# Performance work log

Measured on AMD Instinct MI355X. Metric: run time of the kernel, lower is better.

## Reference

```python
import jax, jax.numpy as jnp
import numpy as np

B, D_IN, T = 16, 1024, 4096
CB_SIZE, CB_DIM = 8192, 512
EPS = 1e-12


def _conv1d_s2(x, w):
    # x: [b, c_in, t], w: [c_out, c_in, 3]; stride 2, padding 1 (matches nn.Conv1d)
    return jax.lax.conv_general_dilated(
        x, w, window_strides=(2,), padding=[(1, 1)],
        dimension_numbers=("NCH", "OIH", "NCH"))


def _l2_normalize(v):
    # F.normalize(v, dim=1) semantics
    return v / jnp.maximum(jnp.linalg.norm(v, axis=1, keepdims=True), EPS)


def setup_inputs() -> dict:
    key = jax.random.key(0)
    k1, k2, k3, k4 = jax.random.split(key, 4)
    x = jax.random.normal(k1, (B, D_IN, T), dtype=jnp.float32)
    w1 = jax.random.normal(k2, (CB_DIM, D_IN, 3), dtype=jnp.float32) * 0.02
    w2 = jax.random.normal(k3, (CB_DIM, CB_DIM, 3), dtype=jnp.float32) * 0.02
    codebook = jax.random.normal(k4, (CB_SIZE, CB_DIM), dtype=jnp.float32)
    return {"x": x, "w1": w1, "w2": w2, "codebook": codebook}


def reference(x, w1, w2, codebook):
    # in_proj: two stride-2 convs -> [b, cb_dim, t], t = T // 4
    x_e = _conv1d_s2(_conv1d_s2(x, w1), w2)
    b, d, t = x_e.shape
    enc = x_e.transpose(0, 2, 1).reshape(b * t, d)   # (b t) d
    enc = _l2_normalize(enc)
    cb = _l2_normalize(codebook)
    # squared euclidean distance via matmul
    dist = (jnp.sum(enc * enc, axis=1, keepdims=True)
            - 2.0 * enc @ cb.T
            + jnp.sum(cb * cb, axis=1)[None, :])     # (b t) codebook_size
    indices = jnp.argmax(-dist, axis=1).reshape(b, t)
    return indices
```

## Files before the change

kernel.cpp:

```cpp
#include <hip/hip_runtime.h>


typedef __attribute__((ext_vector_type(8))) _Float16 f16x8;
typedef __attribute__((ext_vector_type(8))) short bf16x8;
typedef __attribute__((ext_vector_type(4))) float f32x4;

__device__ inline ushort f2bf(float x) {
  union { float f; unsigned u; } v; v.f = x;
  unsigned r = v.u + 0x7fffu + ((v.u >> 16) & 1u);
  return (ushort)(r >> 16);
}

__device__ inline void splitf(float v, ushort& h, ushort& l) {
  union { _Float16 h; ushort u; } a, b;
  a.h = (_Float16)v;
  b.h = (_Float16)(v - (float)a.h);
  h = a.u; l = b.u;
}

__global__ __launch_bounds__(256) void prep_w(const float* __restrict__ w,
                                              ushort* __restrict__ ws,
                                              int n ) {
  const int idx = blockIdx.x * 256 + threadIdx.x;
  if (idx >= n) return;
  const float v0 = w[(size_t)idx * 3 + 0];
  const float v1 = w[(size_t)idx * 3 + 1];
  const float v2 = w[(size_t)idx * 3 + 2];
  ushort h, l;
  splitf(v0, h, l); ws[idx] = h; ws[(size_t)n + idx] = l;
  splitf(v1, h, l); ws[2 * (size_t)n + idx] = h; ws[3 * (size_t)n + idx] = l;
  splitf(v2, h, l); ws[4 * (size_t)n + idx] = h; ws[5 * (size_t)n + idx] = l;
}

__global__ __launch_bounds__(256) void zero_halo(ushort* __restrict__ xo1,
                                                 ushort* __restrict__ xo2) {
  const int b = blockIdx.x, tid = threadIdx.x;
  const uint4 z = make_uint4(0, 0, 0, 0);
  *(uint4*)(xo1 + (size_t)b * 2049 * 2048 + tid * 8) = z;
  if (tid < 128) *(uint4*)(xo2 + (size_t)b * 1025 * 1024 + tid * 8) = z;
}

template <int CI, int T>
__global__ __launch_bounds__(256) void prep_x(const float* __restrict__ x,
                                              ushort* __restrict__ xe,
                                              ushort* __restrict__ xo) {
  const int t0 = blockIdx.x * 256;
  const int ci0 = blockIdx.y * 32;
  const int b = blockIdx.z;
  const int tid = threadIdx.x;
  __shared__ float tile[32][257];
  const int wv = tid >> 6, lane = tid & 63;
  const float* xb = x + ((size_t)b * CI + ci0) * T + t0;
#pragma unroll
  for (int r = 0; r < 8; r++) {
    const int ci = r * 4 + wv;
    const float4 v = *(const float4*)(xb + (size_t)ci * T + lane * 4);
    tile[ci][lane * 4 + 0] = v.x; tile[ci][lane * 4 + 1] = v.y;
    tile[ci][lane * 4 + 2] = v.z; tile[ci][lane * 4 + 3] = v.w;
  }
  __syncthreads();
  const int jj = tid >> 1, ph = tid & 1;
  const int tl = 2 * jj + ph;
  __attribute__((aligned(16))) ushort h[32], l[32];
#pragma unroll
  for (int c = 0; c < 32; c++) splitf(tile[c][tl], h[c], l[c]);
  constexpr int TH = T / 2;
  constexpr int RW = CI * 2;
  ushort* dst;
  if (ph == 0) dst = xe + ((size_t)b * TH + (t0 >> 1) + jj) * RW;
  else dst = xo + ((size_t)b * (TH + 1) + (t0 >> 1) + jj + 1) * RW;
  dst += (ci0 >> 5) * 64;
#pragma unroll
  for (int k = 0; k < 4; k++) {
    *(uint4*)(dst + k * 8) = *(const uint4*)(h + k * 8);
    *(uint4*)(dst + 32 + k * 8) = *(const uint4*)(l + k * 8);
  }
}

template <int C_IN, int T_OUT, bool SPLIT_OUT>
__global__ __launch_bounds__(256, 4) void conv_mfma(
    const ushort* __restrict__ xe, const ushort* __restrict__ xo,
    const ushort* __restrict__ ws, float* __restrict__ out,
    ushort* __restrict__ ye, ushort* __restrict__ yo) {
  const int co0 = blockIdx.x * 128;
  const int t0 = blockIdx.y * 64;
  const int b = blockIdx.z;
  const int tid = threadIdx.x;
  const int wv = tid >> 6, lane = tid & 63;
  const int l15 = lane & 15, quad = lane >> 4;

  __shared__ ushort xeh[64 * 40], xel[64 * 40], xoh[65 * 40], xol[65 * 40];

  f32x4 acc[2][4] = {};
  const int RW = C_IN * 2;
  const ushort* xe_b = xe + ((size_t)b * T_OUT + t0) * RW;
  const ushort* xo_b = xo + ((size_t)b * (T_OUT + 1) + t0) * RW;

  for (int ci0 = 0; ci0 < C_IN; ci0 += 32) {
    __syncthreads();
    const int choff = (ci0 >> 5) * 64;
#pragma unroll
    for (int q = 0; q < 5; q++) {
      const int id = tid + 256 * q;
      if (id < 1032) {
        const int g = id & 3;
        const int u = id >> 2;
        const uint4* src;
        ushort* dst;
        if (u < 128) {
          const int row = u >> 1, part = u & 1;
          src = (const uint4*)(xe_b + (size_t)row * RW + choff + part * 32 + g * 8);
          dst = (part ? xel : xeh) + row * 40 + g * 8;
        } else {
          const int u2 = u - 128;
          const int row = u2 >> 1, part = u2 & 1;
          src = (const uint4*)(xo_b + (size_t)row * RW + choff + part * 32 + g * 8);
          dst = (part ? xol : xoh) + row * 40 + g * 8;
        }
        *(uint4*)dst = *src;
      }
    }
    __syncthreads();

#pragma unroll
    for (int koff = 0; koff < 3; koff++) {
      f16x8 a_h[2], a_l[2];
#pragma unroll
      for (int i = 0; i < 2; i++) {
        const size_t co = (size_t)co0 + wv * 32 + i * 16 + l15;
        const ushort* wp = ws + ((size_t)(koff * 2) * 512) * C_IN + co * C_IN + ci0 + quad * 8;
        a_h[i] = *(const f16x8*)wp;
        a_l[i] = *(const f16x8*)(wp + (size_t)512 * C_IN);
      }
      const ushort* bh = (koff == 1) ? xeh : xoh;
      const ushort* bl = (koff == 1) ? xel : xol;
      const int radd = (koff == 2) ? 1 : 0;
#pragma unroll
      for (int j = 0; j < 4; j++) {
        const int row = j * 16 + l15 + radd;
        const f16x8 b_h = *(const f16x8*)(bh + row * 40 + quad * 8);
        const f16x8 b_l = *(const f16x8*)(bl + row * 40 + quad * 8);
#pragma unroll
        for (int i = 0; i < 2; i++) {
          acc[i][j] = __builtin_amdgcn_mfma_f32_16x16x32_f16(a_h[i], b_h, acc[i][j], 0, 0, 0);
          acc[i][j] = __builtin_amdgcn_mfma_f32_16x16x32_f16(a_h[i], b_l, acc[i][j], 0, 0, 0);
          acc[i][j] = __builtin_amdgcn_mfma_f32_16x16x32_f16(a_l[i], b_h, acc[i][j], 0, 0, 0);
        }
      }
    }
  }

  if (SPLIT_OUT) {
#pragma unroll
    for (int i = 0; i < 2; i++) {
      const int ch = (co0 >> 5) + wv;
      const int ci32 = i * 16 + quad * 4;
#pragma unroll
      for (int j = 0; j < 4; j++) {
        const int t = t0 + j * 16 + l15;
        const int ph = t & 1;
        const int row = (t >> 1) + ph;
        __attribute__((aligned(8))) ushort h[4], l[4];
#pragma unroll
        for (int r = 0; r < 4; r++) splitf(acc[i][j][r], h[r], l[r]);
        ushort* dst = (ph ? yo : ye) +
                      ((size_t)b * (ph ? 1025 : 1024) + row) * 1024 + ch * 64 + ci32;
        *(uint2*)dst = *(const uint2*)h;
        *(uint2*)(dst + 32) = *(const uint2*)l;
      }
    }
  } else {
#pragma unroll
    for (int i = 0; i < 2; i++) {
#pragma unroll
      for (int j = 0; j < 4; j++) {
        const int t = t0 + j * 16 + l15;
        const int co = co0 + wv * 32 + i * 16 + quad * 4;
        const float4 v = make_float4(acc[i][j][0], acc[i][j][1], acc[i][j][2], acc[i][j][3]);
        *(float4*)(out + ((size_t)b * T_OUT + t) * 512 + co) = v;
      }
    }
  }
}

__global__ __launch_bounds__(64) void norm_rows(const float* __restrict__ out2t,
                                                float* __restrict__ enc,
                                                ushort* __restrict__ enc16) {
  const int row = blockIdx.x;
  const int lane = threadIdx.x;
  const float* p = out2t + (size_t)row * 512 + lane * 8;
  const float4 v0 = *(const float4*)p;
  const float4 v1 = *(const float4*)(p + 4);
  float ss = v0.x * v0.x + v0.y * v0.y + v0.z * v0.z + v0.w * v0.w +
             v1.x * v1.x + v1.y * v1.y + v1.z * v1.z + v1.w * v1.w;
#pragma unroll
  for (int m = 32; m >= 1; m >>= 1) ss += __shfl_xor(ss, m, 64);
  const float inv = 1.0f / fmaxf(sqrtf(ss), 1e-12f);
  float4 a, c;
  a.x = v0.x * inv; a.y = v0.y * inv; a.z = v0.z * inv; a.w = v0.w * inv;
  c.x = v1.x * inv; c.y = v1.y * inv; c.z = v1.z * inv; c.w = v1.w * inv;
  float* eo = enc + (size_t)row * 512 + lane * 8;
  *(float4*)eo = a;
  *(float4*)(eo + 4) = c;
  __attribute__((aligned(16))) ushort u[8] = {
      f2bf(a.x), f2bf(a.y), f2bf(a.z), f2bf(a.w),
      f2bf(c.x), f2bf(c.y), f2bf(c.z), f2bf(c.w)};
  *(uint4*)(enc16 + (size_t)row * 512 + lane * 8) = *(const uint4*)u;
}

__global__ __launch_bounds__(256) void norm_cb(const float* __restrict__ cb,
                                               float* __restrict__ cbn,
                                               ushort* __restrict__ cbn16,
                                               float* __restrict__ cb2) {
  const int row = blockIdx.x * 4 + (threadIdx.x >> 6);
  const int lane = threadIdx.x & 63;
  const float* p = cb + (long)row * 512;
  const float4 v0 = *(const float4*)(p + lane * 4);
  const float4 v1 = *(const float4*)(p + 256 + lane * 4);
  float ss = v0.x * v0.x + v0.y * v0.y + v0.z * v0.z + v0.w * v0.w +
             v1.x * v1.x + v1.y * v1.y + v1.z * v1.z + v1.w * v1.w;
#pragma unroll
  for (int m = 32; m >= 1; m >>= 1) ss += __shfl_xor(ss, m, 64);
  const float n = fmaxf(sqrtf(ss), 1e-12f);
  float4 a, c;
  a.x = v0.x / n; a.y = v0.y / n; a.z = v0.z / n; a.w = v0.w / n;
  c.x = v1.x / n; c.y = v1.y / n; c.z = v1.z / n; c.w = v1.w / n;
  *(float4*)(cbn + (long)row * 512 + lane * 4) = a;
  *(float4*)(cbn + (long)row * 512 + 256 + lane * 4) = c;
  ushort4 ua, uc;
  ua.x = f2bf(a.x); ua.y = f2bf(a.y); ua.z = f2bf(a.z); ua.w = f2bf(a.w);
  uc.x = f2bf(c.x); uc.y = f2bf(c.y); uc.z = f2bf(c.z); uc.w = f2bf(c.w);
  *(ushort4*)(cbn16 + (long)row * 512 + lane * 4) = ua;
  *(ushort4*)(cbn16 + (long)row * 512 + 256 + lane * 4) = uc;
  float s2 = a.x * a.x + a.y * a.y + a.z * a.z + a.w * a.w +
             c.x * c.x + c.y * c.y + c.z * c.z + c.w * c.w;
#pragma unroll
  for (int m = 32; m >= 1; m >>= 1) s2 += __shfl_xor(s2, m, 64);
  if (lane == 0) cb2[row] = s2;
}

__device__ inline void top2_merge(float& s1, int& i1, float& s2, int& i2,
                                  float t1, int j1, float t2, int j2) {
  if (t1 > s1) {
    if (s1 > t2) { s2 = s1; i2 = i1; } else { s2 = t2; i2 = j2; }
    s1 = t1; i1 = j1;
  } else if (t1 > s2) {
    s2 = t1; i2 = j1;
  }
}

__global__ __launch_bounds__(256) void score_top2(
    const ushort* __restrict__ enc16, const ushort* __restrict__ cbn16,
    const float* __restrict__ cb2, float* __restrict__ pscore,
    int* __restrict__ pidx) {
  const int nt = blockIdx.x;
  const int mt = blockIdx.y;
  const int m0 = mt * 128, n0 = nt * 128;
  const int tid = threadIdx.x;
  const int wave = tid >> 6, lane = tid & 63;
  const int wm = wave & 1, wn = wave >> 1;
  const int quad = lane >> 4, l15 = lane & 15;

  __shared__ ushort a_s[128 * 72];
  __shared__ ushort b_s[128 * 72];

  f32x4 acc[4][4] = {};

  for (int k0 = 0; k0 < 512; k0 += 64) {
#pragma unroll
    for (int q = 0; q < 4; q++) {
      const int chunk = tid + 256 * q;
      const int row = chunk >> 3, kb = chunk & 7;
      const uint4 va = *(const uint4*)(enc16 + (size_t)(m0 + row) * 512 + k0 + kb * 8);
      *(uint4*)(a_s + row * 72 + kb * 8) = va;
      const uint4 vb = *(const uint4*)(cbn16 + (size_t)(n0 + row) * 512 + k0 + kb * 8);
      *(uint4*)(b_s + row * 72 + kb * 8) = vb;
    }
    __syncthreads();
#pragma unroll
    for (int kk = 0; kk < 2; kk++) {
      bf16x8 af[4], bf[4];
#pragma unroll
      for (int i = 0; i < 4; i++)
        af[i] = *(const bf16x8*)(a_s + (wm * 64 + i * 16 + l15) * 72 + kk * 32 + quad * 8);
#pragma unroll
      for (int j = 0; j < 4; j++)
        bf[j] = *(const bf16x8*)(b_s + (wn * 64 + j * 16 + l15) * 72 + kk * 32 + quad * 8);
#pragma unroll
      for (int i = 0; i < 4; i++)
#pragma unroll
        for (int j = 0; j < 4; j++)
          acc[i][j] = __builtin_amdgcn_mfma_f32_16x16x32_bf16(af[i], bf[j], acc[i][j], 0, 0, 0);
    }
    __syncthreads();
  }

  float cb2c[4];
  int coln[4];
#pragma unroll
  for (int j = 0; j < 4; j++) {
    coln[j] = n0 + wn * 64 + j * 16 + l15;
    cb2c[j] = cb2[coln[j]];
  }

#pragma unroll
  for (int mi = 0; mi < 4; mi++) {
#pragma unroll
    for (int i = 0; i < 4; i++) {
      float s1 = -3.4e38f, s2 = -3.4e38f;
      int i1 = -1, i2 = -1;
#pragma unroll
      for (int j = 0; j < 4; j++) {
        const float s = 2.0f * acc[mi][j][i] - cb2c[j];
        if (s > s1) { s2 = s1; i2 = i1; s1 = s; i1 = coln[j]; }
        else if (s > s2) { s2 = s; i2 = coln[j]; }
      }
#pragma unroll
      for (int m = 8; m >= 1; m >>= 1) {
        const float t1 = __shfl_xor(s1, m, 64);
        const int j1 = __shfl_xor(i1, m, 64);
        const float t2 = __shfl_xor(s2, m, 64);
        const int j2 = __shfl_xor(i2, m, 64);
        top2_merge(s1, i1, s2, i2, t1, j1, t2, j2);
      }
      if (l15 == 0) {
        const int row_g = m0 + wm * 64 + mi * 16 + quad * 4 + i;
        const size_t base = (size_t)row_g * 256 + (size_t)nt * 4 + wn * 2;
        pscore[base] = s1; pidx[base] = i1;
        pscore[base + 1] = s2; pidx[base + 1] = i2;
      }
    }
  }
}

__global__ __launch_bounds__(256) void rescore_argmax(
    const float* __restrict__ enc, const float* __restrict__ cbn,
    const float* __restrict__ cb2, const float* __restrict__ pscore,
    const int* __restrict__ pidx, int* __restrict__ out) {
  const int row = blockIdx.x;
  const int tid = threadIdx.x;
  __shared__ float wbest[4];
  __shared__ int wslot[4];
  __shared__ int winner;
  __shared__ int cand[8];
  __shared__ float fsc[8];
  __shared__ int fid[8];

  float s = pscore[(size_t)row * 256 + tid];
  const int id = pidx[(size_t)row * 256 + tid];

  for (int it = 0; it < 8; it++) {
    float bs = s;
    int bslot = tid;
#pragma unroll
    for (int m = 32; m >= 1; m >>= 1) {
      const float os = __shfl_xor(bs, m, 64);
      const int oslot = __shfl_xor(bslot, m, 64);
      if (os > bs || (os == bs && oslot < bslot)) { bs = os; bslot = oslot; }
    }
    if ((tid & 63) == 0) { wbest[tid >> 6] = bs; wslot[tid >> 6] = bslot; }
    __syncthreads();
    if (tid == 0) {
      float b = wbest[0]; int sl = wslot[0];
      for (int wv = 1; wv < 4; wv++)
        if (wbest[wv] > b || (wbest[wv] == b && wslot[wv] < sl)) { b = wbest[wv]; sl = wslot[wv]; }
      winner = sl;
    }
    __syncthreads();
    if (tid == winner) { cand[it] = id; s = -3.4e38f; }
    __syncthreads();
  }

  const int c = cand[tid >> 5];
  const float* ep = enc + (size_t)row * 512;
  const float* cp = cbn + (size_t)c * 512;
  float dot = 0.0f;
  const int d0 = (tid & 31) * 16;
#pragma unroll
  for (int u = 0; u < 4; u++) {
    const float4 e4 = *(const float4*)(ep + d0 + u * 4);
    const float4 c4 = *(const float4*)(cp + d0 + u * 4);
    dot = fmaf(e4.x, c4.x, dot);
    dot = fmaf(e4.y, c4.y, dot);
    dot = fmaf(e4.z, c4.z, dot);
    dot = fmaf(e4.w, c4.w, dot);
  }
#pragma unroll
  for (int m = 16; m >= 1; m >>= 1) dot += __shfl_xor(dot, m, 64);
  if ((tid & 31) == 0) {
    fsc[tid >> 5] = 2.0f * dot - cb2[c];
    fid[tid >> 5] = c;
  }
  __syncthreads();
  if (tid == 0) {
    float b = fsc[0]; int bi = fid[0];
    for (int q = 1; q < 8; q++)
      if (fsc[q] > b || (fsc[q] == b && fid[q] < bi)) { b = fsc[q]; bi = fid[q]; }
    out[row] = bi;
  }
}

extern "C" void kernel_launch(void* const* d_in, const int* in_sizes, int n_in,
                              void* d_out, int out_size, void* d_ws, size_t ws_size,
                              hipStream_t stream) {
  const float* x = (const float*)d_in[0];
  const float* w1 = (const float*)d_in[1];
  const float* w2 = (const float*)d_in[2];
  const float* cb = (const float*)d_in[3];
  int* out = (int*)d_out;

  char* w0 = (char*)d_ws;
  const size_t MB = 1ull << 20;
  ushort* xe1 = (ushort*)(w0);
  ushort* xo1 = (ushort*)(w0 + 128 * MB);
  ushort* xe2 = (ushort*)(w0 + 257 * MB);
  ushort* xo2 = (ushort*)(w0 + 289 * MB);
  ushort* ws1 = (ushort*)(w0 + 322 * MB);
  ushort* ws2 = (ushort*)(w0 + 328 * MB);
  float* out2t = (float*)(w0);
  float* enc = (float*)(w0 + 32 * MB);
  ushort* enc16 = (ushort*)(w0 + 64 * MB);
  float* cbn = (float*)(w0 + 80 * MB);
  ushort* cbn16 = (ushort*)(w0 + 96 * MB);
  float* cb2 = (float*)(w0 + 104 * MB);
  float* pscore = (float*)(w0 + 112 * MB);
  int* pidx = (int*)(w0 + 128 * MB);

  zero_halo<<<16, 256, 0, stream>>>(xo1, xo2);
  prep_w<<<2048, 256, 0, stream>>>(w1, ws1, 512 * 1024);
  prep_w<<<1024, 256, 0, stream>>>(w2, ws2, 512 * 512);
  prep_x<1024, 4096><<<dim3(16, 32, 16), 256, 0, stream>>>(x, xe1, xo1);
  conv_mfma<1024, 2048, true><<<dim3(4, 32, 16), 256, 0, stream>>>(
      xe1, xo1, ws1, nullptr, xe2, xo2);
  conv_mfma<512, 1024, false><<<dim3(4, 16, 16), 256, 0, stream>>>(
      xe2, xo2, ws2, out2t, nullptr, nullptr);
  norm_rows<<<16384, 64, 0, stream>>>(out2t, enc, enc16);
  norm_cb<<<2048, 256, 0, stream>>>(cb, cbn, cbn16, cb2);
  score_top2<<<dim3(64, 128), 256, 0, stream>>>(enc16, cbn16, cb2, pscore, pidx);
  rescore_argmax<<<16384, 256, 0, stream>>>(enc, cbn, cb2, pscore, pidx, out);
}
```

Baseline: 1.751 ms.

## Load score tiles via global_load_lds with XOR-swizzled bf16 layout

The score kernel now stages A and B tiles with direct global-to-LDS loads (global_load_lds, 16 bytes per lane) instead of going through registers, which drops the padded LDS rows. To avoid bank conflicts without padding, the producer kernels write enc16 and cbn16 in an XOR-swizzled 8-element-group order, and the MFMA fragment reads undo that swizzle. This saves register traffic and LDS space but ties the global layout to the swizzle, and any other consumer of enc16/cbn16 must use the same layout.

```diff
diff --git a/kernel.cpp b/kernel.cpp
--- a/kernel.cpp
+++ b/kernel.cpp
@@ -16,6 +16,12 @@
   a.h = (_Float16)v;
   b.h = (_Float16)(v - (float)a.h);
   h = a.u; l = b.u;
+}
+
+__device__ inline void gload_lds16(const ushort* g, ushort* l) {
+  __builtin_amdgcn_global_load_lds(
+      (const __attribute__((address_space(1))) unsigned int*)g,
+      (__attribute__((address_space(3))) unsigned int*)l, 16, 0, 0);
 }
 
 __global__ __launch_bounds__(256) void prep_w(const float* __restrict__ w,
@@ -205,7 +211,8 @@
   __attribute__((aligned(16))) ushort u[8] = {
       f2bf(a.x), f2bf(a.y), f2bf(a.z), f2bf(a.w),
       f2bf(c.x), f2bf(c.y), f2bf(c.z), f2bf(c.w)};
-  *(uint4*)(enc16 + (size_t)row * 512 + lane * 8) = *(const uint4*)u;
+  const int sidx = (lane & 56) | ((lane ^ row) & 7);
+  *(uint4*)(enc16 + (size_t)row * 512 + sidx * 8) = *(const uint4*)u;
 }
 
 __global__ __launch_bounds__(256) void norm_cb(const float* __restrict__ cb,
@@ -230,8 +237,12 @@
   ushort4 ua, uc;
   ua.x = f2bf(a.x); ua.y = f2bf(a.y); ua.z = f2bf(a.z); ua.w = f2bf(a.w);
   uc.x = f2bf(c.x); uc.y = f2bf(c.y); uc.z = f2bf(c.z); uc.w = f2bf(c.w);
-  *(ushort4*)(cbn16 + (long)row * 512 + lane * 4) = ua;
-  *(ushort4*)(cbn16 + (long)row * 512 + 256 + lane * 4) = uc;
+  const int idx0 = lane * 4;
+  const int idx1 = 256 + lane * 4;
+  const int s0 = (idx0 & ~56) | ((((idx0 >> 3) ^ row) & 7) << 3);
+  const int s1 = (idx1 & ~56) | ((((idx1 >> 3) ^ row) & 7) << 3);
+  *(ushort4*)(cbn16 + (long)row * 512 + s0) = ua;
+  *(ushort4*)(cbn16 + (long)row * 512 + s1) = uc;
   float s2 = a.x * a.x + a.y * a.y + a.z * a.z + a.w * a.w +
              c.x * c.x + c.y * c.y + c.z * c.z + c.w * c.w;
 #pragma unroll
@@ -261,38 +272,47 @@
   const int wm = wave & 1, wn = wave >> 1;
   const int quad = lane >> 4, l15 = lane & 15;
 
-  __shared__ ushort a_s[128 * 72];
-  __shared__ ushort b_s[128 * 72];
+  __shared__ __attribute__((aligned(16))) ushort a_s[128 * 64];
+  __shared__ __attribute__((aligned(16))) ushort b_s[128 * 64];
 
   f32x4 acc[4][4] = {};
 
+  const int srow = lane >> 3;
+  const int sgrp = lane & 7;
+  const ushort* ag = enc16 + ((size_t)(m0 + wave * 32 + srow) * 512) + sgrp * 8;
+  const ushort* bg = cbn16 + ((size_t)(n0 + wave * 32 + srow) * 512) + sgrp * 8;
+  ushort* al = a_s + (wave * 32 + srow) * 64;
+  ushort* bl = b_s + (wave * 32 + srow) * 64;
+  (void)al; (void)bl;
+
   for (int k0 = 0; k0 < 512; k0 += 64) {
-#pragma unroll
-    for (int q = 0; q < 4; q++) {
-      const int chunk = tid + 256 * q;
-      const int row = chunk >> 3, kb = chunk & 7;
-      const uint4 va = *(const uint4*)(enc16 + (size_t)(m0 + row) * 512 + k0 + kb * 8);
-      *(uint4*)(a_s + row * 72 + kb * 8) = va;
-      const uint4 vb = *(const uint4*)(cbn16 + (size_t)(n0 + row) * 512 + k0 + kb * 8);
-      *(uint4*)(b_s + row * 72 + kb * 8) = vb;
-    }
-    __syncthreads();
+    __syncthreads();
+#pragma unroll
+    for (int it = 0; it < 4; it++) {
+      gload_lds16(ag + (size_t)(it * 8) * 512 + k0, a_s + (wave * 32 + it * 8) * 64);
+      gload_lds16(bg + (size_t)(it * 8) * 512 + k0, b_s + (wave * 32 + it * 8) * 64);
+    }
+    __syncthreads();
+
 #pragma unroll
     for (int kk = 0; kk < 2; kk++) {
       bf16x8 af[4], bf[4];
 #pragma unroll
-      for (int i = 0; i < 4; i++)
-        af[i] = *(const bf16x8*)(a_s + (wm * 64 + i * 16 + l15) * 72 + kk * 32 + quad * 8);
-#pragma unroll
-      for (int j = 0; j < 4; j++)
-        bf[j] = *(const bf16x8*)(b_s + (wn * 64 + j * 16 + l15) * 72 + kk * 32 + quad * 8);
+      for (int i = 0; i < 4; i++) {
+        const int r = wm * 64 + i * 16 + l15;
+        af[i] = *(const bf16x8*)(a_s + r * 64 + (((kk * 4 + quad) ^ (l15 & 7)) * 8));
+      }
+#pragma unroll
+      for (int j = 0; j < 4; j++) {
+        const int r = wn * 64 + j * 16 + l15;
+        bf[j] = *(const bf16x8*)(b_s + r * 64 + (((kk * 4 + quad) ^ (l15 & 7)) * 8));
+      }
 #pragma unroll
       for (int i = 0; i < 4; i++)
 #pragma unroll
         for (int j = 0; j < 4; j++)
           acc[i][j] = __builtin_amdgcn_mfma_f32_16x16x32_bf16(af[i], bf[j], acc[i][j], 0, 0, 0);
     }
-    __syncthreads();
   }
 
   float cb2c[4];
```

New measurement: 1.733 ms. About the same (-1.1%).
